# Optimization experiments

Measured on AMD Instinct MI355X. Metric: run time of the kernel, lower is better.

The kernel has to match this reference:

```python
import jax, jax.numpy as jnp
import numpy as np

NUM_EMBEDDINGS = 2048
BATCH_SIZE = 8
SEQ_LEN = 512
SPATIAL_DIM = 1024
EMBED_DIM = BATCH_SIZE * SEQ_LEN  # 4096
COMMITMENT_COST = 0.25


def setup_inputs() -> dict:
    key = jax.random.key(0)
    k1, k2 = jax.random.split(key)
    inputs = jax.random.normal(k1, (BATCH_SIZE, SEQ_LEN, SPATIAL_DIM), dtype=jnp.float32)
    # original init: uniform(-1/K, 1/K); scaled normal is an acceptable stand-in scale
    embedding = jax.random.uniform(k2, (NUM_EMBEDDINGS, EMBED_DIM), dtype=jnp.float32,
                                   minval=-1.0 / NUM_EMBEDDINGS, maxval=1.0 / NUM_EMBEDDINGS)
    return {"inputs": inputs, "embedding": embedding}


def reference(inputs, embedding):
    B, L, S = inputs.shape
    K, D = embedding.shape
    sg = jax.lax.stop_gradient
    # [S, D] : one feature vector per spatial feature index
    x = jnp.transpose(inputs, (2, 0, 1)).reshape(S, -1)
    # squared-euclidean distances via expansion (avoids S x K x D intermediate)
    d = (jnp.sum(x * x, axis=1, keepdims=True)
         - 2.0 * jnp.einsum('sd,kd->sk', x, embedding)
         + jnp.sum(embedding * embedding, axis=1)[None, :])  # [S, K]
    idx = jnp.argmin(d, axis=1)                 # [S]
    q = embedding[idx]                          # [S, D] gather == one_hot @ E
    # per-feature losses (mse over the (1, D) feature vector == mean over D)
    e_latent = jnp.mean((sg(q) - x) ** 2, axis=1)
    q_latent = jnp.mean((q - sg(x)) ** 2, axis=1)
    total_loss = jnp.mean(q_latent + COMMITMENT_COST * e_latent)
    # straight-through estimator
    q_ste = x + sg(q - x)
    quantized_output = jnp.transpose(q_ste.reshape(S, B, L), (1, 2, 0))  # [B, L, S]
    # per-feature perplexity: encodings is (1, K) one-hot, avg over dim0 is the row itself
    enc = jax.nn.one_hot(idx, K, dtype=x.dtype)  # [S, K]
    perpl = jnp.exp(-jnp.sum(enc * jnp.log(enc + 1e-10), axis=1))  # [S]
    avg_perplexity = jnp.mean(perpl)
    return (total_loss, quantized_output, avg_perplexity, idx)
```

## Files before the change

kernel.cpp:

```cpp
#include <hip/hip_runtime.h>
#include <hip/hip_bf16.h>
#include <math.h>

#define S_DIM 1024
#define K_DIM 2048
#define D_DIM 4096

#define OUT_Q    1
#define OUT_PERP (1 + D_DIM * S_DIM)
#define OUT_IDX  (2 + D_DIM * S_DIM)

#define MARGIN 6.0e-3f
#define CONF_GAP 4.5e-3f
#define FLT_BIG 3.4028235e38f

#define WS_LOSS   0
#define WS_XX     64
#define WS_EE     4160
#define WS_MINP   77888
#define WS_CNT    143424
#define WS_IDX    208960
#define WS_KCAND  213056
#define WS_SCAND  2310208
#define WS_ESTAGE 4407360
#define WS_XSTAGE 21184576
#define WS_BEST   29573184
#define WS_PAIRS  29581376
#define WS_EEP    30105664ull
#define WS_XXP2   31154240ull
#define WS_NEEDED3 31678528ull

#define FB_LOSS 0
#define FB_XX   4096
#define FB_EE   8192
#define FB_XXP  16384
#define FB_MINV 81920
#define FB_MINI 212992
#define FB_IDX  344064

typedef __attribute__((ext_vector_type(8))) short bf16x8;
typedef __attribute__((ext_vector_type(4))) float f32x4;

__device__ __forceinline__ unsigned short f2bf(float f) {
    __hip_bfloat16 h = __float2bfloat16(f);
    return *reinterpret_cast<unsigned short*>(&h);
}

__device__ __forceinline__ void gload16(const void* g, void* l) {
    __builtin_amdgcn_global_load_lds(
        (const __attribute__((address_space(1))) unsigned int*)(g),
        (__attribute__((address_space(3))) unsigned int*)(l), 16, 0, 0);
}

__global__ __launch_bounds__(256) void k_xx_part(const float* __restrict__ A, float* __restrict__ xxp) {
    const int dc = blockIdx.x;
    const int s = blockIdx.y * 256 + threadIdx.x;
    float acc = 0.f;
    for (int dd = 0; dd < 256; ++dd) {
        const int d = dc * 256 + dd;
        float v = A[(size_t)d * S_DIM + s];
        acc = fmaf(v, v, acc);
    }
    xxp[dc * S_DIM + s] = acc;
}

__global__ __launch_bounds__(256) void k_xx_comb(const float* __restrict__ xxp, float* __restrict__ xx) {
    const int s = blockIdx.x * 256 + threadIdx.x;
    float acc = 0.f;
    for (int dc = 0; dc < 16; ++dc) acc += xxp[dc * S_DIM + s];
    xx[s] = acc;
}

__global__ __launch_bounds__(256) void k_ee(const float* __restrict__ E, float* __restrict__ ee) {
    const int k = blockIdx.x;
    const float4* row = (const float4*)(E + (size_t)k * D_DIM);
    float acc = 0.f;
#pragma unroll
    for (int j = 0; j < 4; ++j) {
        float4 v = row[threadIdx.x + j * 256];
        acc = fmaf(v.x, v.x, acc);
        acc = fmaf(v.y, v.y, acc);
        acc = fmaf(v.z, v.z, acc);
        acc = fmaf(v.w, v.w, acc);
    }
    __shared__ float red[256];
    red[threadIdx.x] = acc;
    __syncthreads();
    for (int off = 128; off > 0; off >>= 1) {
        if (threadIdx.x < off) red[threadIdx.x] += red[threadIdx.x + off];
        __syncthreads();
    }
    if (threadIdx.x == 0) ee[k] = red[0];
}

__global__ __launch_bounds__(256) void k_convE(const float* __restrict__ E, char* __restrict__ Estage,
                                               float* __restrict__ eep) {
    const int dt = blockIdx.x;
    const int kt = blockIdx.y;
    const int tid = threadIdx.x;
    char* tile = Estage + (size_t)kt * 1048576 + (size_t)dt * 8192;
#pragma unroll
    for (int i = 0; i < 2; ++i) {
        int idx = i * 256 + tid;
        int row = idx >> 2, dc = idx & 3;
        const float4* src = (const float4*)(E + (size_t)(kt * 128 + row) * D_DIM + dt * 32 + dc * 8);
        float4 v0 = src[0], v1 = src[1];
        float vals[8] = {v0.x, v0.y, v0.z, v0.w, v1.x, v1.y, v1.z, v1.w};
        unsigned int w[4];
#pragma unroll
        for (int q = 0; q < 4; ++q)
            w[q] = (unsigned int)f2bf(vals[2 * q]) | ((unsigned int)f2bf(vals[2 * q + 1]) << 16);
        int c_dst = ((row >> 6) * 4 + ((row >> 4) & 3)) * 64 + dc * 16 + (row & 15);
        *(uint4*)(tile + (size_t)c_dst * 16) = make_uint4(w[0], w[1], w[2], w[3]);
        float p = 0.f;
#pragma unroll
        for (int q = 0; q < 8; ++q) p = fmaf(vals[q], vals[q], p);
        p += __shfl_down(p, 2);
        p += __shfl_down(p, 1);
        if ((tid & 3) == 0) eep[(size_t)dt * K_DIM + kt * 128 + row] = p;
    }
}

__global__ __launch_bounds__(256) void k_convX(const float* __restrict__ A, float* __restrict__ AT,
                                               char* __restrict__ Xstage, float* __restrict__ xxp2) {
    __shared__ float ldsT[32][65];
    const int dt = blockIdx.x;
    const int st = blockIdx.y;
    const int tid = threadIdx.x;
#pragma unroll
    for (int i = 0; i < 2; ++i) {
        int idx = i * 256 + tid;
        int row_d = idx >> 4, c = idx & 15;
        float4 v = *(const float4*)(A + (size_t)(dt * 32 + row_d) * S_DIM + st * 64 + c * 4);
        ldsT[row_d][c * 4 + 0] = v.x;
        ldsT[row_d][c * 4 + 1] = v.y;
        ldsT[row_d][c * 4 + 2] = v.z;
        ldsT[row_d][c * 4 + 3] = v.w;
    }
    __syncthreads();
    {
        int s_row = tid >> 2, dpart = (tid & 3) * 8;
        float vals[8];
#pragma unroll
        for (int j = 0; j < 8; ++j) vals[j] = ldsT[dpart + j][s_row];
        float* dst = AT + (size_t)(st * 64 + s_row) * D_DIM + dt * 32 + dpart;
        *(float4*)(dst + 0) = make_float4(vals[0], vals[1], vals[2], vals[3]);
        *(float4*)(dst + 4) = make_float4(vals[4], vals[5], vals[6], vals[7]);
        float p = 0.f;
#pragma unroll
        for (int j = 0; j < 8; ++j) p = fmaf(vals[j], vals[j], p);
        p += __shfl_down(p, 2);
        p += __shfl_down(p, 1);
        if ((tid & 3) == 0) xxp2[(size_t)dt * S_DIM + st * 64 + s_row] = p;
    }
    {
        int s_row = tid >> 2, dc = tid & 3;
        float vals[8];
#pragma unroll
        for (int j = 0; j < 8; ++j) vals[j] = ldsT[dc * 8 + j][s_row];
        unsigned int w[4];
#pragma unroll
        for (int q = 0; q < 4; ++q)
            w[q] = (unsigned int)f2bf(vals[2 * q]) | ((unsigned int)f2bf(vals[2 * q + 1]) << 16);
        int gn = ((s_row >> 5) << 1) | ((s_row >> 4) & 1);
        int c_dst = gn * 64 + dc * 16 + (s_row & 15);
        char* tile = Xstage + (size_t)st * 524288 + (size_t)dt * 4096;
        *(uint4*)(tile + (size_t)c_dst * 16) = make_uint4(w[0], w[1], w[2], w[3]);
    }
}

__global__ __launch_bounds__(256) void k_sums(const float* __restrict__ eep, const float* __restrict__ xxp2,
                                              float* __restrict__ ee, float* __restrict__ xx) {
    const int gid = blockIdx.x * 256 + threadIdx.x;
    if (gid < K_DIM) {
        float a = 0.f;
        for (int dt = 0; dt < 128; ++dt) a += eep[(size_t)dt * K_DIM + gid];
        ee[gid] = a;
    } else if (gid < K_DIM + S_DIM) {
        const int s = gid - K_DIM;
        float a = 0.f;
        for (int dt = 0; dt < 128; ++dt) a += xxp2[(size_t)dt * S_DIM + s];
        xx[s] = a;
    }
}

__global__ __launch_bounds__(512) void k_gemm_score4(const char* __restrict__ Estage, const char* __restrict__ Xstage,
                                                     const float* __restrict__ xx, const float* __restrict__ ee,
                                                     float* __restrict__ minp, int* __restrict__ cnt,
                                                     int* __restrict__ kcand, float* __restrict__ scand) {
    __shared__ short lds[2 * 6 * 6144];
    __shared__ float minw[2][64];
    __shared__ float minb[64];
    __shared__ int cntl[64];

    const int linear = blockIdx.y * 16 + blockIdx.x;
    const int wsw = (linear & 7) * 32 + (linear >> 3);
    const int st = wsw & 15;
    const int ktb = wsw >> 4;

    const int tid = threadIdx.x;
    const int h = tid >> 8;
    const int tidh = tid & 255;
    const int wid2 = tidh >> 6;
    const int wm = wid2 >> 1;
    const int wn = wid2 & 1;
    const int lane = tid & 63;
    const int lr = lane & 15;
    const int lh = lane >> 4;

    const char* Eb = Estage + (size_t)ktb * 1048576;
    const char* Xb = Xstage + (size_t)st * 524288;
    short* myl = lds + h * 36864;

    f32x4 acc[4][2];
#pragma unroll
    for (int f = 0; f < 4; ++f)
#pragma unroll
        for (int g = 0; g < 2; ++g) acc[f][g] = (f32x4){0.f, 0.f, 0.f, 0.f};

#define STG(t, sl) { \
    const char* eb_ = Eb + (size_t)(h * 64 + (t)) * 8192; \
    char* d_ = (char*)myl + (sl) * 12288; \
    gload16(eb_ + tidh * 16, d_ + tidh * 16); \
    gload16(eb_ + 4096 + tidh * 16, d_ + 4096 + tidh * 16); \
    gload16(Xb + (size_t)(h * 64 + (t)) * 4096 + tidh * 16, d_ + 8192 + tidh * 16); }

#define CMP(sl) { \
    const short* s_ = myl + (sl) * 6144; \
    bf16x8 af[4], bx[2]; \
    _Pragma("unroll") \
    for (int f = 0; f < 4; ++f) af[f] = *(const bf16x8*)(s_ + (wm * 4 + f) * 512 + lane * 8); \
    _Pragma("unroll") \
    for (int g = 0; g < 2; ++g) bx[g] = *(const bf16x8*)(s_ + 4096 + (wn * 2 + g) * 512 + lane * 8); \
    _Pragma("unroll") \
    for (int f = 0; f < 4; ++f) { \
        _Pragma("unroll") \
        for (int g = 0; g < 2; ++g) \
            acc[f][g] = __builtin_amdgcn_mfma_f32_16x16x32_bf16(af[f], bx[g], acc[f][g], 0, 0, 0); \
    } }

#define WB(nstr) asm volatile("s_waitcnt vmcnt(" nstr ")\n\ts_barrier" ::: "memory")
#define BAR asm volatile("s_barrier" ::: "memory")

    STG(0, 0) STG(1, 1) STG(2, 2) STG(3, 3) STG(4, 4)

    for (int bb = 0; bb < 54; bb += 6) {
        STG(bb + 5, 5)  WB("15"); CMP(0) BAR;
        STG(bb + 6, 0)  WB("15"); CMP(1) BAR;
        STG(bb + 7, 1)  WB("15"); CMP(2) BAR;
        STG(bb + 8, 2)  WB("15"); CMP(3) BAR;
        STG(bb + 9, 3)  WB("15"); CMP(4) BAR;
        STG(bb + 10, 4) WB("15"); CMP(5) BAR;
    }
    STG(59, 5) WB("15"); CMP(0) BAR;
    STG(60, 0) WB("15"); CMP(1) BAR;
    STG(61, 1) WB("15"); CMP(2) BAR;
    STG(62, 2) WB("15"); CMP(3) BAR;
    STG(63, 3) WB("15"); CMP(4) BAR;
    WB("12"); CMP(5) BAR;
    WB("9");  CMP(0) BAR;
    WB("6");  CMP(1) BAR;
    WB("3");  CMP(2) BAR;
    WB("0");  CMP(3)
    __syncthreads();

#undef STG
#undef CMP
#undef WB
#undef BAR

    f32x4* red4 = (f32x4*)lds;
    if (h == 1) {
#pragma unroll
        for (int f = 0; f < 4; ++f)
#pragma unroll
            for (int g = 0; g < 2; ++g) red4[(f * 2 + g) * 256 + tidh] = acc[f][g];
    }
    __syncthreads();
    if (h == 0) {
#pragma unroll
        for (int f = 0; f < 4; ++f)
#pragma unroll
            for (int g = 0; g < 2; ++g) acc[f][g] += red4[(f * 2 + g) * 256 + tidh];
    }

    float xs[2], ek[4][4];
#pragma unroll
    for (int g = 0; g < 2; ++g) xs[g] = xx[st * 64 + wn * 32 + g * 16 + lr];
#pragma unroll
    for (int f = 0; f < 4; ++f)
#pragma unroll
        for (int r = 0; r < 4; ++r) ek[f][r] = ee[ktb * 128 + wm * 64 + f * 16 + lh * 4 + r];

    float mg[2] = {FLT_BIG, FLT_BIG};
#pragma unroll
    for (int f = 0; f < 4; ++f)
#pragma unroll
        for (int g = 0; g < 2; ++g)
#pragma unroll
            for (int r = 0; r < 4; ++r) {
                float sc = (xs[g] - 2.0f * acc[f][g][r]) + ek[f][r];
                mg[g] = fminf(mg[g], sc);
            }
#pragma unroll
    for (int g = 0; g < 2; ++g) {
        mg[g] = fminf(mg[g], __shfl_xor(mg[g], 16));
        mg[g] = fminf(mg[g], __shfl_xor(mg[g], 32));
    }
    if (h == 0 && lane < 16) {
        minw[wm][wn * 32 + lane] = mg[0];
        minw[wm][wn * 32 + 16 + lane] = mg[1];
    }
    __syncthreads();
    if (tid < 64) {
        float mb = fminf(minw[0][tid], minw[1][tid]);
        minb[tid] = mb;
        minp[ktb * S_DIM + st * 64 + tid] = mb;
        cntl[tid] = 0;
    }
    __syncthreads();
    if (h == 0) {
#pragma unroll
        for (int f = 0; f < 4; ++f)
#pragma unroll
            for (int g = 0; g < 2; ++g)
#pragma unroll
                for (int r = 0; r < 4; ++r) {
                    float sc = (xs[g] - 2.0f * acc[f][g][r]) + ek[f][r];
                    int sl = wn * 32 + g * 16 + lr;
                    if (sc <= minb[sl] + MARGIN) {
                        int slot = atomicAdd(&cntl[sl], 1);
                        if (slot < 32) {
                            int si = ktb * S_DIM + st * 64 + sl;
                            kcand[si * 32 + slot] = ktb * 128 + wm * 64 + f * 16 + lh * 4 + r;
                            scand[si * 32 + slot] = sc;
                        }
                    }
                }
    }
    __syncthreads();
    if (tid < 64) cnt[ktb * S_DIM + st * 64 + tid] = min(cntl[tid], 32);
}

__global__ __launch_bounds__(64) void k_select_gate(const float* __restrict__ minp, const int* __restrict__ cnt,
                                                    const int* __restrict__ kcand, const float* __restrict__ scand,
                                                    int* __restrict__ idx, float* __restrict__ out,
                                                    int* __restrict__ npairs, int2* __restrict__ pairs) {
    __shared__ int   lcand[64];
    __shared__ float lsc[64];
    __shared__ int   lcount;
    const int s = blockIdx.x;
    const int lane = threadIdx.x;
    if (lane == 0) lcount = 0;

    float mv = (lane < 16) ? minp[lane * S_DIM + s] : FLT_BIG;
#pragma unroll
    for (int off = 1; off < 64; off <<= 1) mv = fminf(mv, __shfl_xor(mv, off));
    const float m_a = mv;

    int myc = (lane < 16) ? cnt[lane * S_DIM + s] : 0;
    float gsc[16]; int gkc[16]; int gcs[16];
#pragma unroll
    for (int kt = 0; kt < 16; ++kt) {
        int c = __shfl(myc, kt);
        gcs[kt] = c;
        gsc[kt] = FLT_BIG; gkc[kt] = 0;
        if (lane < c) {
            gsc[kt] = scand[(kt * S_DIM + s) * 32 + lane];
            gkc[kt] = kcand[(kt * S_DIM + s) * 32 + lane];
        }
    }
#pragma unroll
    for (int kt = 0; kt < 16; ++kt) {
        if (lane < gcs[kt] && gsc[kt] <= m_a + MARGIN) {
            int slot = atomicAdd(&lcount, 1);
            if (slot < 64) { lcand[slot] = gkc[kt]; lsc[slot] = gsc[kt]; }
        }
    }
    __syncthreads();
    const int n = min(lcount, 64);

    float bv = (lane < n) ? lsc[lane] : FLT_BIG;
    int   bk = (lane < n) ? lcand[lane] : 0x7fffffff;
#pragma unroll
    for (int off = 1; off < 64; off <<= 1) {
        float ov = __shfl_xor(bv, off); int ok = __shfl_xor(bk, off);
        if (ov < bv || (ov == bv && ok < bk)) { bv = ov; bk = ok; }
    }
    float sv = (lane < n && lcand[lane] != bk) ? lsc[lane] : FLT_BIG;
#pragma unroll
    for (int off = 1; off < 64; off <<= 1) sv = fminf(sv, __shfl_xor(sv, off));

    if (n == 1 || sv - bv > CONF_GAP) {
        if (lane == 0) { idx[s] = bk; out[OUT_IDX + s] = (float)bk; }
        return;
    }

    bool em = (lane < n) && (lsc[lane] <= bv + CONF_GAP);
    unsigned long long m = __ballot(em);
    int cnt2 = __popcll(m);
    int base = 0;
    if (lane == 0) base = atomicAdd(npairs, cnt2);
    base = __shfl(base, 0);
    int off2 = (int)__popcll(m & ((1ull << lane) - 1ull));
    if (em) pairs[base + off2] = make_int2(s, lcand[lane]);
}

__global__ __launch_bounds__(64) void k_pair_chain(const float* __restrict__ AT, const float* __restrict__ E,
                                                   const float* __restrict__ xx, const float* __restrict__ ee,
                                                   const int* __restrict__ npairs, const int2* __restrict__ pairs,
                                                   unsigned long long* __restrict__ best) {
    const int np = min(*npairs, 65536);
    const int lane = threadIdx.x;
    for (int p = blockIdx.x; p < np; p += gridDim.x) {
        int2 pr = pairs[p];
        const float4* er4 = (const float4*)(E + (size_t)pr.y * D_DIM) + lane * 16;
        const float4* xr4 = (const float4*)(AT + (size_t)pr.x * D_DIM) + lane * 16;
        float4 er[16], xr[16];
#pragma unroll
        for (int i = 0; i < 16; ++i) { er[i] = er4[i]; xr[i] = xr4[i]; }

        float c = 0.f;
        for (int seg = 0; seg < 64; ++seg) {
            float cin = __shfl(c, (seg + 63) & 63);
            if (lane == seg) {
                float a = (seg == 0) ? 0.f : cin;
#pragma unroll
                for (int i = 0; i < 16; ++i) {
                    a = fmaf(er[i].x, xr[i].x, a);
                    a = fmaf(er[i].y, xr[i].y, a);
                    a = fmaf(er[i].z, xr[i].z, a);
                    a = fmaf(er[i].w, xr[i].w, a);
                }
                c = a;
            }
        }
        float dot = __shfl(c, 63);
        if (lane == 0) {
            float u = xx[pr.x] - 2.0f * dot;
            float sc = u + ee[pr.y];
            unsigned long long pk = ((unsigned long long)__float_as_uint(sc) << 32) | (unsigned int)pr.y;
            atomicMin(&best[pr.x], pk);
        }
    }
}

__global__ __launch_bounds__(256) void k_select_fin(const unsigned long long* __restrict__ best,
                                                    int* __restrict__ idx, float* __restrict__ out) {
    const int s = blockIdx.x * 256 + threadIdx.x;
    unsigned long long b = best[s];
    if (b != 0xFFFFFFFFFFFFFFFFull) {
        int k = (int)(b & 0xFFFFFFFFu);
        idx[s] = k;
        out[OUT_IDX + s] = (float)k;
    }
}

__global__ __launch_bounds__(256) void k_gemm_argmin(const float* __restrict__ A, const float* __restrict__ E,
                                                     const float* __restrict__ xx, const float* __restrict__ ee,
                                                     float* __restrict__ minv, int* __restrict__ mini) {
    __shared__ float Et[32][64];
    __shared__ float At[32][64];
    __shared__ float rv[16][64];
    __shared__ int   ri[16][64];
    const int kt = blockIdx.x, st = blockIdx.y;
    const int k0 = kt * 64, s0 = st * 64;
    const int tid = threadIdx.x;
    const int tcol = tid & 15, trow = tid >> 4;
    float acc[4][4] = {{0.f,0.f,0.f,0.f},{0.f,0.f,0.f,0.f},{0.f,0.f,0.f,0.f},{0.f,0.f,0.f,0.f}};
    for (int dt = 0; dt < D_DIM / 32; ++dt) {
        const int d0 = dt * 32;
        __syncthreads();
#pragma unroll
        for (int it = 0; it < 2; ++it) {
            int f = tid + it * 256;
            int kk = f >> 3, dd4 = f & 7;
            float4 v = *(const float4*)(E + (size_t)(k0 + kk) * D_DIM + d0 + dd4 * 4);
            Et[dd4 * 4 + 0][kk] = v.x; Et[dd4 * 4 + 1][kk] = v.y;
            Et[dd4 * 4 + 2][kk] = v.z; Et[dd4 * 4 + 3][kk] = v.w;
        }
#pragma unroll
        for (int it = 0; it < 2; ++it) {
            int f = tid + it * 256;
            int ss4 = f & 15, dd = f >> 4;
            float4 v = *(const float4*)(A + (size_t)(d0 + dd) * S_DIM + s0 + ss4 * 4);
            *(float4*)&At[dd][ss4 * 4] = v;
        }
        __syncthreads();
#pragma unroll 8
        for (int dd = 0; dd < 32; ++dd) {
            float4 a4 = *(const float4*)&At[dd][tcol * 4];
            float4 e4 = *(const float4*)&Et[dd][trow * 4];
            float a[4] = {a4.x, a4.y, a4.z, a4.w};
            float e[4] = {e4.x, e4.y, e4.z, e4.w};
#pragma unroll
            for (int i = 0; i < 4; ++i)
#pragma unroll
                for (int j = 0; j < 4; ++j) acc[i][j] = fmaf(e[i], a[j], acc[i][j]);
        }
    }
    float xs[4], ek[4];
#pragma unroll
    for (int j = 0; j < 4; ++j) xs[j] = xx[s0 + tcol * 4 + j];
#pragma unroll
    for (int i = 0; i < 4; ++i) ek[i] = ee[k0 + trow * 4 + i];
#pragma unroll
    for (int j = 0; j < 4; ++j) {
        float bv = FLT_BIG; int bk = 0x7fffffff;
#pragma unroll
        for (int i = 0; i < 4; ++i) {
            float xe = acc[i][j];
            float u = xs[j] - 2.0f * xe;
            float sc = u + ek[i];
            int k = k0 + trow * 4 + i;
            if (sc < bv) { bv = sc; bk = k; }
        }
        rv[trow][tcol * 4 + j] = bv;
        ri[trow][tcol * 4 + j] = bk;
    }
    __syncthreads();
    if (tid < 64) {
        float bv = rv[0][tid]; int bk = ri[0][tid];
#pragma unroll
        for (int r = 1; r < 16; ++r) {
            float v = rv[r][tid]; int k2 = ri[r][tid];
            if (v < bv || (v == bv && k2 < bk)) { bv = v; bk = k2; }
        }
        minv[kt * S_DIM + s0 + tid] = bv;
        mini[kt * S_DIM + s0 + tid] = bk;
    }
}

__global__ __launch_bounds__(256) void k_argmin_final(const float* __restrict__ minv, const int* __restrict__ mini,
                                                      int* __restrict__ idx, float* __restrict__ out) {
    const int s = blockIdx.x * 256 + threadIdx.x;
    float bv = minv[s];
    int bk = mini[s];
    for (int kt = 1; kt < 32; ++kt) {
        float v = minv[kt * S_DIM + s];
        int k2 = mini[kt * S_DIM + s];
        if (v < bv || (v == bv && k2 < bk)) { bv = v; bk = k2; }
    }
    idx[s] = bk;
    out[OUT_IDX + s] = (float)bk;
}

__global__ __launch_bounds__(256) void k_output_loss(const float* __restrict__ A, const float* __restrict__ E,
                                                     const int* __restrict__ idx, float* __restrict__ out,
                                                     float* __restrict__ loss) {
    __shared__ float qt[64][65];
    __shared__ int sidx[64];
    __shared__ float red[256];
    const int st = blockIdx.x, dtb = blockIdx.y;
    const int s0 = st * 64, d0 = dtb * 64;
    const int tid = threadIdx.x;
    if (tid < 64) sidx[tid] = idx[s0 + tid];
    __syncthreads();
#pragma unroll
    for (int it = 0; it < 4; ++it) {
        int f = tid + it * 256;
        int si = f >> 4, c4 = f & 15;
        float4 v = *(const float4*)(E + (size_t)sidx[si] * D_DIM + d0 + c4 * 4);
        qt[si][c4 * 4 + 0] = v.x; qt[si][c4 * 4 + 1] = v.y;
        qt[si][c4 * 4 + 2] = v.z; qt[si][c4 * 4 + 3] = v.w;
    }
    __syncthreads();
    const int ss = tid & 63;
    const int dg = tid >> 6;
    float lsum = 0.f;
#pragma unroll
    for (int i = 0; i < 16; ++i) {
        const int dd = dg * 16 + i;
        const int d = d0 + dd;
        float x = A[(size_t)d * S_DIM + s0 + ss];
        float q = qt[ss][dd];
        float diff = q - x;
        float val = x + diff;
        out[OUT_Q + (size_t)d * S_DIM + s0 + ss] = val;
        lsum = fmaf(diff, diff, lsum);
    }
    red[tid] = lsum;
    __syncthreads();
    for (int off = 128; off > 0; off >>= 1) {
        if (tid < off) red[tid] += red[tid + off];
        __syncthreads();
    }
    if (tid == 0) atomicAdd(loss, red[0]);
}

__global__ void k_scalars(const float* __restrict__ loss, float* __restrict__ out) {
    out[0] = 1.25f * loss[0] * (1.0f / (float)(S_DIM * D_DIM));
    out[OUT_PERP] = 1.0f;
}

extern "C" void kernel_launch(void* const* d_in, const int* in_sizes, int n_in,
                              void* d_out, int out_size, void* d_ws, size_t ws_size,
                              hipStream_t stream) {
    const float* A = (const float*)d_in[0];
    const float* E = (const float*)d_in[1];
    float* out = (float*)d_out;
    char* ws = (char*)d_ws;

    if (ws_size >= WS_NEEDED3) {
        float* w_loss = (float*)(ws + WS_LOSS);
        int*   w_np   = (int*)(ws + 16);
        float* w_xx   = (float*)(ws + WS_XX);
        float* w_ee   = (float*)(ws + WS_EE);
        float* w_minp = (float*)(ws + WS_MINP);
        int*   w_cnt  = (int*)(ws + WS_CNT);
        int*   w_idx  = (int*)(ws + WS_IDX);
        int*   w_kc   = (int*)(ws + WS_KCAND);
        float* w_sc   = (float*)(ws + WS_SCAND);
        char*  w_es   = ws + WS_ESTAGE;
        char*  w_xs   = ws + WS_XSTAGE;
        unsigned long long* w_best = (unsigned long long*)(ws + WS_BEST);
        int2*  w_pairs = (int2*)(ws + WS_PAIRS);
        float* w_eep  = (float*)(ws + WS_EEP);
        float* w_xxp2 = (float*)(ws + WS_XXP2);
        float* AT     = out + OUT_Q;

        hipMemsetAsync(ws, 0, 64, stream);
        hipMemsetAsync(ws + WS_BEST, 0xFF, 8192, stream);
        k_convE<<<dim3(128, 16), 256, 0, stream>>>(E, w_es, w_eep);
        k_convX<<<dim3(128, 16), 256, 0, stream>>>(A, AT, w_xs, w_xxp2);
        k_sums<<<dim3(12), 256, 0, stream>>>(w_eep, w_xxp2, w_ee, w_xx);
        k_gemm_score4<<<dim3(16, 16), 512, 0, stream>>>(w_es, w_xs, w_xx, w_ee, w_minp, w_cnt, w_kc, w_sc);
        k_select_gate<<<dim3(S_DIM), 64, 0, stream>>>(w_minp, w_cnt, w_kc, w_sc, w_idx, out, w_np, w_pairs);
        k_pair_chain<<<dim3(2048), 64, 0, stream>>>(AT, E, w_xx, w_ee, w_np, w_pairs, w_best);
        k_select_fin<<<dim3(4), 256, 0, stream>>>(w_best, w_idx, out);
        k_output_loss<<<dim3(16, 64), 256, 0, stream>>>(A, E, w_idx, out, w_loss);
        k_scalars<<<1, 1, 0, stream>>>(w_loss, out);
    } else {
        float* w_loss = (float*)(ws + FB_LOSS);
        float* w_xx   = (float*)(ws + FB_XX);
        float* w_ee   = (float*)(ws + FB_EE);
        float* w_xxp  = (float*)(ws + FB_XXP);
        float* w_minv = (float*)(ws + FB_MINV);
        int*   w_mini = (int*)(ws + FB_MINI);
        int*   w_idx  = (int*)(ws + FB_IDX);

        hipMemsetAsync(ws, 0, 256, stream);
        k_xx_part<<<dim3(16, 4), 256, 0, stream>>>(A, w_xxp);
        k_ee<<<dim3(K_DIM), 256, 0, stream>>>(E, w_ee);
        k_xx_comb<<<dim3(4), 256, 0, stream>>>(w_xxp, w_xx);
        k_gemm_argmin<<<dim3(32, 16), 256, 0, stream>>>(A, E, w_xx, w_ee, w_minv, w_mini);
        k_argmin_final<<<dim3(4), 256, 0, stream>>>(w_minv, w_mini, w_idx, out);
        k_output_loss<<<dim3(16, 64), 256, 0, stream>>>(A, E, w_idx, out, w_loss);
        k_scalars<<<1, 1, 0, stream>>>(w_loss, out);
    }
}
```

Before: 117.1 us.

## Split GEMM K-loop across four wave groups and merge conversion kernels

The scoring GEMM now runs 1024 threads per block, with four groups each handling a quarter of the reduction dimension, using a 3-slot load pipeline per group instead of 6 slots for two groups. Partial accumulators are reduced through LDS into group zero. The E and X conversion kernels are merged into one launch with a doubled grid. This is intended to increase in-block parallelism and latency hiding and to drop a launch, at the cost of a shallower prefetch pipeline and a larger cross-group reduction.

```diff
diff --git a/kernel.cpp b/kernel.cpp
--- a/kernel.cpp
+++ b/kernel.cpp
@@ -93,79 +93,78 @@
     if (threadIdx.x == 0) ee[k] = red[0];
 }
 
-__global__ __launch_bounds__(256) void k_convE(const float* __restrict__ E, char* __restrict__ Estage,
-                                               float* __restrict__ eep) {
-    const int dt = blockIdx.x;
-    const int kt = blockIdx.y;
-    const int tid = threadIdx.x;
-    char* tile = Estage + (size_t)kt * 1048576 + (size_t)dt * 8192;
-#pragma unroll
-    for (int i = 0; i < 2; ++i) {
-        int idx = i * 256 + tid;
-        int row = idx >> 2, dc = idx & 3;
-        const float4* src = (const float4*)(E + (size_t)(kt * 128 + row) * D_DIM + dt * 32 + dc * 8);
-        float4 v0 = src[0], v1 = src[1];
-        float vals[8] = {v0.x, v0.y, v0.z, v0.w, v1.x, v1.y, v1.z, v1.w};
-        unsigned int w[4];
-#pragma unroll
-        for (int q = 0; q < 4; ++q)
-            w[q] = (unsigned int)f2bf(vals[2 * q]) | ((unsigned int)f2bf(vals[2 * q + 1]) << 16);
-        int c_dst = ((row >> 6) * 4 + ((row >> 4) & 3)) * 64 + dc * 16 + (row & 15);
-        *(uint4*)(tile + (size_t)c_dst * 16) = make_uint4(w[0], w[1], w[2], w[3]);
-        float p = 0.f;
-#pragma unroll
-        for (int q = 0; q < 8; ++q) p = fmaf(vals[q], vals[q], p);
-        p += __shfl_down(p, 2);
-        p += __shfl_down(p, 1);
-        if ((tid & 3) == 0) eep[(size_t)dt * K_DIM + kt * 128 + row] = p;
-    }
-}
-
-__global__ __launch_bounds__(256) void k_convX(const float* __restrict__ A, float* __restrict__ AT,
-                                               char* __restrict__ Xstage, float* __restrict__ xxp2) {
+__global__ __launch_bounds__(256) void k_conv(const float* __restrict__ E, const float* __restrict__ A,
+                                              float* __restrict__ AT, char* __restrict__ Estage,
+                                              char* __restrict__ Xstage, float* __restrict__ eep,
+                                              float* __restrict__ xxp2) {
     __shared__ float ldsT[32][65];
     const int dt = blockIdx.x;
-    const int st = blockIdx.y;
     const int tid = threadIdx.x;
-#pragma unroll
-    for (int i = 0; i < 2; ++i) {
-        int idx = i * 256 + tid;
-        int row_d = idx >> 4, c = idx & 15;
-        float4 v = *(const float4*)(A + (size_t)(dt * 32 + row_d) * S_DIM + st * 64 + c * 4);
-        ldsT[row_d][c * 4 + 0] = v.x;
-        ldsT[row_d][c * 4 + 1] = v.y;
-        ldsT[row_d][c * 4 + 2] = v.z;
-        ldsT[row_d][c * 4 + 3] = v.w;
-    }
-    __syncthreads();
-    {
-        int s_row = tid >> 2, dpart = (tid & 3) * 8;
-        float vals[8];
-#pragma unroll
-        for (int j = 0; j < 8; ++j) vals[j] = ldsT[dpart + j][s_row];
-        float* dst = AT + (size_t)(st * 64 + s_row) * D_DIM + dt * 32 + dpart;
-        *(float4*)(dst + 0) = make_float4(vals[0], vals[1], vals[2], vals[3]);
-        *(float4*)(dst + 4) = make_float4(vals[4], vals[5], vals[6], vals[7]);
-        float p = 0.f;
-#pragma unroll
-        for (int j = 0; j < 8; ++j) p = fmaf(vals[j], vals[j], p);
-        p += __shfl_down(p, 2);
-        p += __shfl_down(p, 1);
-        if ((tid & 3) == 0) xxp2[(size_t)dt * S_DIM + st * 64 + s_row] = p;
-    }
-    {
-        int s_row = tid >> 2, dc = tid & 3;
-        float vals[8];
-#pragma unroll
-        for (int j = 0; j < 8; ++j) vals[j] = ldsT[dc * 8 + j][s_row];
-        unsigned int w[4];
-#pragma unroll
-        for (int q = 0; q < 4; ++q)
-            w[q] = (unsigned int)f2bf(vals[2 * q]) | ((unsigned int)f2bf(vals[2 * q + 1]) << 16);
-        int gn = ((s_row >> 5) << 1) | ((s_row >> 4) & 1);
-        int c_dst = gn * 64 + dc * 16 + (s_row & 15);
-        char* tile = Xstage + (size_t)st * 524288 + (size_t)dt * 4096;
-        *(uint4*)(tile + (size_t)c_dst * 16) = make_uint4(w[0], w[1], w[2], w[3]);
+    if (blockIdx.y < 16) {
+        const int kt = blockIdx.y;
+        char* tile = Estage + (size_t)kt * 1048576 + (size_t)dt * 8192;
+#pragma unroll
+        for (int i = 0; i < 2; ++i) {
+            int idx = i * 256 + tid;
+            int row = idx >> 2, dc = idx & 3;
+            const float4* src = (const float4*)(E + (size_t)(kt * 128 + row) * D_DIM + dt * 32 + dc * 8);
+            float4 v0 = src[0], v1 = src[1];
+            float vals[8] = {v0.x, v0.y, v0.z, v0.w, v1.x, v1.y, v1.z, v1.w};
+            unsigned int w[4];
+#pragma unroll
+            for (int q = 0; q < 4; ++q)
+                w[q] = (unsigned int)f2bf(vals[2 * q]) | ((unsigned int)f2bf(vals[2 * q + 1]) << 16);
+            int c_dst = ((row >> 6) * 4 + ((row >> 4) & 3)) * 64 + dc * 16 + (row & 15);
+            *(uint4*)(tile + (size_t)c_dst * 16) = make_uint4(w[0], w[1], w[2], w[3]);
+            float p = 0.f;
+#pragma unroll
+            for (int q = 0; q < 8; ++q) p = fmaf(vals[q], vals[q], p);
+            p += __shfl_down(p, 2);
+            p += __shfl_down(p, 1);
+            if ((tid & 3) == 0) eep[(size_t)dt * K_DIM + kt * 128 + row] = p;
+        }
+    } else {
+        const int st = blockIdx.y - 16;
+#pragma unroll
+        for (int i = 0; i < 2; ++i) {
+            int idx = i * 256 + tid;
+            int row_d = idx >> 4, c = idx & 15;
+            float4 v = *(const float4*)(A + (size_t)(dt * 32 + row_d) * S_DIM + st * 64 + c * 4);
+            ldsT[row_d][c * 4 + 0] = v.x;
+            ldsT[row_d][c * 4 + 1] = v.y;
+            ldsT[row_d][c * 4 + 2] = v.z;
+            ldsT[row_d][c * 4 + 3] = v.w;
+        }
+        __syncthreads();
+        {
+            int s_row = tid >> 2, dpart = (tid & 3) * 8;
+            float vals[8];
+#pragma unroll
+            for (int j = 0; j < 8; ++j) vals[j] = ldsT[dpart + j][s_row];
+            float* dst = AT + (size_t)(st * 64 + s_row) * D_DIM + dt * 32 + dpart;
+            *(float4*)(dst + 0) = make_float4(vals[0], vals[1], vals[2], vals[3]);
+            *(float4*)(dst + 4) = make_float4(vals[4], vals[5], vals[6], vals[7]);
+            float p = 0.f;
+#pragma unroll
+            for (int j = 0; j < 8; ++j) p = fmaf(vals[j], vals[j], p);
+            p += __shfl_down(p, 2);
+            p += __shfl_down(p, 1);
+            if ((tid & 3) == 0) xxp2[(size_t)dt * S_DIM + st * 64 + s_row] = p;
+        }
+        {
+            int s_row = tid >> 2, dc = tid & 3;
+            float vals[8];
+#pragma unroll
+            for (int j = 0; j < 8; ++j) vals[j] = ldsT[dc * 8 + j][s_row];
+            unsigned int w[4];
+#pragma unroll
+            for (int q = 0; q < 4; ++q)
+                w[q] = (unsigned int)f2bf(vals[2 * q]) | ((unsigned int)f2bf(vals[2 * q + 1]) << 16);
+            int gn = ((s_row >> 5) << 1) | ((s_row >> 4) & 1);
+            int c_dst = gn * 64 + dc * 16 + (s_row & 15);
+            char* tile = Xstage + (size_t)st * 524288 + (size_t)dt * 4096;
+            *(uint4*)(tile + (size_t)c_dst * 16) = make_uint4(w[0], w[1], w[2], w[3]);
+        }
     }
 }
 
@@ -184,11 +183,11 @@
     }
 }
 
-__global__ __launch_bounds__(512) void k_gemm_score4(const char* __restrict__ Estage, const char* __restrict__ Xstage,
-                                                     const float* __restrict__ xx, const float* __restrict__ ee,
-                                                     float* __restrict__ minp, int* __restrict__ cnt,
-                                                     int* __restrict__ kcand, float* __restrict__ scand) {
-    __shared__ short lds[2 * 6 * 6144];
+__global__ __launch_bounds__(1024) void k_gemm_score5(const char* __restrict__ Estage, const char* __restrict__ Xstage,
+                                                      const float* __restrict__ xx, const float* __restrict__ ee,
+                                                      float* __restrict__ minp, int* __restrict__ cnt,
+                                                      int* __restrict__ kcand, float* __restrict__ scand) {
+    __shared__ short lds[4 * 3 * 6144];
     __shared__ float minw[2][64];
     __shared__ float minb[64];
     __shared__ int cntl[64];
@@ -210,7 +209,7 @@
 
     const char* Eb = Estage + (size_t)ktb * 1048576;
     const char* Xb = Xstage + (size_t)st * 524288;
-    short* myl = lds + h * 36864;
+    short* myl = lds + h * 18432;
 
     f32x4 acc[4][2];
 #pragma unroll
@@ -219,11 +218,11 @@
         for (int g = 0; g < 2; ++g) acc[f][g] = (f32x4){0.f, 0.f, 0.f, 0.f};
 
 #define STG(t, sl) { \
-    const char* eb_ = Eb + (size_t)(h * 64 + (t)) * 8192; \
+    const char* eb_ = Eb + (size_t)(h * 32 + (t)) * 8192; \
     char* d_ = (char*)myl + (sl) * 12288; \
     gload16(eb_ + tidh * 16, d_ + tidh * 16); \
     gload16(eb_ + 4096 + tidh * 16, d_ + 4096 + tidh * 16); \
-    gload16(Xb + (size_t)(h * 64 + (t)) * 4096 + tidh * 16, d_ + 8192 + tidh * 16); }
+    gload16(Xb + (size_t)(h * 32 + (t)) * 4096 + tidh * 16, d_ + 8192 + tidh * 16); }
 
 #define CMP(sl) { \
     const short* s_ = myl + (sl) * 6144; \
@@ -242,26 +241,15 @@
 #define WB(nstr) asm volatile("s_waitcnt vmcnt(" nstr ")\n\ts_barrier" ::: "memory")
 #define BAR asm volatile("s_barrier" ::: "memory")
 
-    STG(0, 0) STG(1, 1) STG(2, 2) STG(3, 3) STG(4, 4)
-
-    for (int bb = 0; bb < 54; bb += 6) {
-        STG(bb + 5, 5)  WB("15"); CMP(0) BAR;
-        STG(bb + 6, 0)  WB("15"); CMP(1) BAR;
-        STG(bb + 7, 1)  WB("15"); CMP(2) BAR;
-        STG(bb + 8, 2)  WB("15"); CMP(3) BAR;
-        STG(bb + 9, 3)  WB("15"); CMP(4) BAR;
-        STG(bb + 10, 4) WB("15"); CMP(5) BAR;
-    }
-    STG(59, 5) WB("15"); CMP(0) BAR;
-    STG(60, 0) WB("15"); CMP(1) BAR;
-    STG(61, 1) WB("15"); CMP(2) BAR;
-    STG(62, 2) WB("15"); CMP(3) BAR;
-    STG(63, 3) WB("15"); CMP(4) BAR;
-    WB("12"); CMP(5) BAR;
-    WB("9");  CMP(0) BAR;
-    WB("6");  CMP(1) BAR;
-    WB("3");  CMP(2) BAR;
-    WB("0");  CMP(3)
+    STG(0, 0) STG(1, 1)
+
+    for (int bb = 0; bb < 30; bb += 3) {
+        STG(bb + 2, 2) WB("6"); CMP(0) BAR;
+        STG(bb + 3, 0) WB("6"); CMP(1) BAR;
+        STG(bb + 4, 1) WB("6"); CMP(2) BAR;
+    }
+    WB("3"); CMP(0) BAR;
+    WB("0"); CMP(1)
     __syncthreads();
 
 #undef STG
@@ -270,18 +258,22 @@
 #undef BAR
 
     f32x4* red4 = (f32x4*)lds;
-    if (h == 1) {
+    if (h != 0) {
 #pragma unroll
         for (int f = 0; f < 4; ++f)
 #pragma unroll
-            for (int g = 0; g < 2; ++g) red4[(f * 2 + g) * 256 + tidh] = acc[f][g];
+            for (int g = 0; g < 2; ++g)
+                red4[(size_t)(h - 1) * 2048 + (f * 2 + g) * 256 + tidh] = acc[f][g];
     }
     __syncthreads();
     if (h == 0) {
 #pragma unroll
-        for (int f = 0; f < 4; ++f)
-#pragma unroll
-            for (int g = 0; g < 2; ++g) acc[f][g] += red4[(f * 2 + g) * 256 + tidh];
+        for (int q = 1; q < 4; ++q)
+#pragma unroll
+            for (int f = 0; f < 4; ++f)
+#pragma unroll
+                for (int g = 0; g < 2; ++g)
+                    acc[f][g] += red4[(size_t)(q - 1) * 2048 + (f * 2 + g) * 256 + tidh];
     }
 
     float xs[2], ek[4][4];
@@ -621,10 +613,9 @@
 
         hipMemsetAsync(ws, 0, 64, stream);
         hipMemsetAsync(ws + WS_BEST, 0xFF, 8192, stream);
-        k_convE<<<dim3(128, 16), 256, 0, stream>>>(E, w_es, w_eep);
-        k_convX<<<dim3(128, 16), 256, 0, stream>>>(A, AT, w_xs, w_xxp2);
+        k_conv<<<dim3(128, 32), 256, 0, stream>>>(E, A, AT, w_es, w_xs, w_eep, w_xxp2);
         k_sums<<<dim3(12), 256, 0, stream>>>(w_eep, w_xxp2, w_ee, w_xx);
-        k_gemm_score4<<<dim3(16, 16), 512, 0, stream>>>(w_es, w_xs, w_xx, w_ee, w_minp, w_cnt, w_kc, w_sc);
+        k_gemm_score5<<<dim3(16, 16), 1024, 0, stream>>>(w_es, w_xs, w_xx, w_ee, w_minp, w_cnt, w_kc, w_sc);
         k_select_gate<<<dim3(S_DIM), 64, 0, stream>>>(w_minp, w_cnt, w_kc, w_sc, w_idx, out, w_np, w_pairs);
         k_pair_chain<<<dim3(2048), 64, 0, stream>>>(AT, E, w_xx, w_ee, w_np, w_pairs, w_best);
         k_select_fin<<<dim3(4), 256, 0, stream>>>(w_best, w_idx, out);
```

Measured after the change: 116.6 us. About the same (-0.4%).
